# Kernel tuning notes

Hardware: AMD Instinct MI355X
Metric: run time of the kernel (lower is better)

Reference implementation:

```python
import jax, jax.numpy as jnp
import numpy as np

L, B, S, D, F, E, V, H = 4, 4, 1024, 768, 3072, 4, 256, 12
DH = D // H
TOPK = 2


def _ln(x, g, b, eps=1e-5):
    m = x.mean(-1, keepdims=True)
    v = ((x - m) ** 2).mean(-1, keepdims=True)
    return (x - m) * jax.lax.rsqrt(v + eps) * g + b


def setup_inputs() -> dict:
    key = jax.random.key(0)
    ks = iter(jax.random.split(key, 40))
    w = lambda shape, s=0.02: jax.random.normal(next(ks), shape, jnp.float32) * s
    inp = {
        'text': jax.random.randint(next(ks), (B, S), 0, V),
        'embed': w((V, D)),
        'conv_w': w((D, D, 3)),
        'conv_b': jnp.zeros((D,), jnp.float32),
        'Wq': w((L, D, D)), 'bq': jnp.zeros((L, D), jnp.float32),
        'Wk': w((L, D, D)), 'bk': jnp.zeros((L, D), jnp.float32),
        'Wv': w((L, D, D)), 'bv': jnp.zeros((L, D), jnp.float32),
        'Wo': w((L, D, D)), 'bo': jnp.zeros((L, D), jnp.float32),
        'rw': w((L, D, E)), 'rb': jnp.zeros((L, E), jnp.float32),
        'ew1': w((L, E, D, F)), 'eb1': jnp.zeros((L, E, F), jnp.float32),
        'ew2': w((L, E, F, D)), 'eb2': jnp.zeros((L, E, D), jnp.float32),
        'ln1g': jnp.ones((L, D), jnp.float32), 'ln1b': jnp.zeros((L, D), jnp.float32),
        'ln2g': jnp.ones((L, D), jnp.float32), 'ln2b': jnp.zeros((L, D), jnp.float32),
        'lnfg': jnp.ones((D,), jnp.float32), 'lnfb': jnp.zeros((D,), jnp.float32),
        'outw': w((D, V)), 'outb': jnp.zeros((V,), jnp.float32),
    }
    return inp


def _forward(text, embed, conv_w, conv_b, Wq, bq, Wk, bk, Wv, bv, Wo, bo,
             rw, rb, ew1, eb1, ew2, eb2, ln1g, ln1b, ln2g, ln2b, lnfg, lnfb, outw, outb):
    # --- morfo-semantic tokenizer: embedding + depthwise-ish conv1d residual ---
    x = embed[text]  # [B,S,D]
    xt = x.transpose(0, 2, 1)  # [B,D,S]
    y = jax.lax.conv_general_dilated(xt, conv_w, (1,), 'SAME',
                                     dimension_numbers=('NCH', 'OIH', 'NCH'))
    x = x + jax.nn.gelu(y.transpose(0, 2, 1) + conv_b)

    scale = 1.0 / np.sqrt(DH).astype(np.float32)
    for i in range(L):
        # --- multi-head self-attention (pre-norm residual) ---
        h = _ln(x, ln1g[i], ln1b[i])
        q = (h @ Wq[i] + bq[i]).reshape(B, S, H, DH).transpose(0, 2, 1, 3)
        k = (h @ Wk[i] + bk[i]).reshape(B, S, H, DH).transpose(0, 2, 1, 3)
        v = (h @ Wv[i] + bv[i]).reshape(B, S, H, DH).transpose(0, 2, 1, 3)
        a = jax.nn.softmax(jnp.einsum('bhqd,bhkd->bhqk', q, k) * scale, axis=-1)
        o = jnp.einsum('bhqk,bhkd->bhqd', a, v).transpose(0, 2, 1, 3).reshape(B, S, D)
        x = x + (o @ Wo[i] + bo[i])

        # --- top-2 mixture-of-experts (pre-norm residual) ---
        h = _ln(x, ln2g[i], ln2b[i]).reshape(B * S, D)  # [T,D]
        probs = jax.nn.softmax(h @ rw[i] + rb[i], axis=-1)  # [T,E]
        topv, topi = jax.lax.top_k(probs, TOPK)  # [T,2]
        gate_w = topv / topv.sum(-1, keepdims=True)  # renormalized top-k gates
        gate = (jax.nn.one_hot(topi, E, dtype=h.dtype) * gate_w[..., None]).sum(1)  # [T,E]
        h1 = jax.nn.gelu(jnp.einsum('td,edf->tef', h, ew1[i]) + eb1[i])  # [T,E,F]
        h2 = jnp.einsum('tef,efd->ted', h1, ew2[i]) + eb2[i]  # [T,E,D]
        moe_out = jnp.einsum('te,ted->td', gate, h2)
        x = x + moe_out.reshape(B, S, D)

    x = _ln(x, lnfg, lnfb)
    return x @ outw + outb  # logits [B,S,V]


def reference(text, embed, conv_w, conv_b, Wq, bq, Wk, bk, Wv, bv, Wo, bo,
              rw, rb, ew1, eb1, ew2, eb2, ln1g, ln1b, ln2g, ln2b, lnfg, lnfb, outw, outb):
    return _forward(text, embed, conv_w, conv_b, Wq, bq, Wk, bk, Wv, bv, Wo, bo,
                    rw, rb, ew1, eb1, ew2, eb2, ln1g, ln1b, ln2g, ln2b, lnfg, lnfb, outw, outb)
```

## Files before the change

### kernel.cpp

```cpp
#include <hip/hip_runtime.h>
#include <math.h>

#define L_ 4
#define B_ 4
#define S_ 1024
#define D_ 768
#define F_ 3072
#define E_ 4
#define V_ 256
#define H_ 12
#define DH_ 64
#define T_ (B_*S_)
#define QKV_LD (3*D_)

typedef __attribute__((ext_vector_type(8))) __bf16 bf16x8;
typedef __attribute__((ext_vector_type(4))) float f32x4;
typedef __attribute__((ext_vector_type(8))) unsigned short u16x8;

__device__ __forceinline__ ushort f2bf(float x) {
    union { float f; unsigned int u; } c; c.f = x;
    unsigned int u = c.u;
    unsigned int r = (u + 0x7fffu + ((u >> 16) & 1u)) >> 16;
    return (ushort)r;
}
__device__ __forceinline__ float bf2f(ushort u) {
    union { unsigned int u; float f; } c; c.u = ((unsigned int)u) << 16;
    return c.f;
}
__device__ __forceinline__ void split3(float v, ushort& h, ushort& l, ushort& q) {
    h = f2bf(v);
    float r1 = v - bf2f(h);
    l = f2bf(r1);
    float r2 = r1 - bf2f(l);
    q = f2bf(r2);
}

__device__ __forceinline__ float gelu_f(float x) {
    return 0.5f * x * (1.f + tanhf(0.7978845608028654f * (x + 0.044715f * x * x * x)));
}

__global__ __launch_bounds__(256) void embed_pad_k(const int* __restrict__ text,
                                                   const float* __restrict__ embed,
                                                   ushort* __restrict__ xpH,
                                                   ushort* __restrict__ xpL,
                                                   ushort* __restrict__ xpQ) {
    int idx = blockIdx.x * 256 + threadIdx.x;
    const int tot = B_ * (S_ + 2) * D_;
    if (idx >= tot) return;
    int d = idx % D_;
    int sp = (idx / D_) % (S_ + 2);
    int b = idx / (D_ * (S_ + 2));
    float v = 0.f;
    if (sp >= 1 && sp <= S_) {
        int tok = text[b * S_ + sp - 1];
        v = embed[(long)tok * D_ + d];
    }
    ushort h, l, q; split3(v, h, l, q);
    xpH[idx] = h; xpL[idx] = l; xpQ[idx] = q;
}

__global__ __launch_bounds__(256) void repack_conv_k(const float* __restrict__ w,
                                                     ushort* __restrict__ cH,
                                                     ushort* __restrict__ cL,
                                                     ushort* __restrict__ cQ) {
    int idx = blockIdx.x * 256 + threadIdx.x;
    if (idx >= D_ * 3 * D_) return;
    int o = idx / (3 * D_);
    int r = idx % (3 * D_);
    int wi = r / D_;
    int i = r % D_;
    float v = w[((long)o * D_ + i) * 3 + wi];
    ushort h, l, q; split3(v, h, l, q);
    cH[idx] = h; cL[idx] = l; cQ[idx] = q;
}

__global__ __launch_bounds__(256) void conv_rows_k(int* __restrict__ r) {
    int t = blockIdx.x * 256 + threadIdx.x;
    if (t < T_) r[t] = t + 2 * (t / S_);
}

__global__ void zero_cnt_k(int* c) { if (threadIdx.x < L_ * E_) c[threadIdx.x] = 0; }

__global__ void concat3_k(const float* __restrict__ a, const float* __restrict__ b,
                          const float* __restrict__ c, float* __restrict__ o) {
    int t = blockIdx.x * 256 + threadIdx.x;
    if (t < D_) o[t] = a[t];
    else if (t < 2 * D_) o[t] = b[t - D_];
    else if (t < 3 * D_) o[t] = c[t - 2 * D_];
}

__global__ __launch_bounds__(256) void tr4_split_k(const float* __restrict__ s0,
                                                   const float* __restrict__ s1,
                                                   const float* __restrict__ s2,
                                                   const float* __restrict__ s3,
                                                   ushort* __restrict__ dH,
                                                   ushort* __restrict__ dL,
                                                   ushort* __restrict__ dQ,
                                                   int K, int N, long dstStride) {
    int z = blockIdx.z;
    const float* src = (z == 0) ? s0 : (z == 1) ? s1 : (z == 2) ? s2 : s3;
    dH += (long)z * dstStride;
    dL += (long)z * dstStride;
    dQ += (long)z * dstStride;
    __shared__ float tile[32][33];
    int tx = threadIdx.x & 31, ty = threadIdx.x >> 5;
    int n = blockIdx.x * 32 + tx;
    int k0 = blockIdx.y * 32;
    #pragma unroll
    for (int r = ty; r < 32; r += 8)
        tile[r][tx] = src[(long)(k0 + r) * N + n];
    __syncthreads();
    int k = k0 + tx;
    long nb = (long)blockIdx.x * 32;
    #pragma unroll
    for (int r = ty; r < 32; r += 8) {
        float v = tile[tx][r];
        ushort h, l, q; split3(v, h, l, q);
        dH[(nb + r) * K + k] = h;
        dL[(nb + r) * K + k] = l;
        dQ[(nb + r) * K + k] = q;
    }
}

__global__ __launch_bounds__(256) void ln_k(const float* __restrict__ x,
                                            const float* __restrict__ g,
                                            const float* __restrict__ bb,
                                            ushort* __restrict__ oH,
                                            ushort* __restrict__ oL,
                                            ushort* __restrict__ oQ) {
    __shared__ float red[256];
    int row = blockIdx.x, tid = threadIdx.x;
    const float* xr = x + (long)row * D_;
    float v0 = xr[tid], v1 = xr[tid + 256], v2 = xr[tid + 512];
    red[tid] = v0 + v1 + v2; __syncthreads();
    for (int off = 128; off; off >>= 1) { if (tid < off) red[tid] += red[tid + off]; __syncthreads(); }
    float mean = red[0] * (1.f / D_);
    __syncthreads();
    float d0 = v0 - mean, d1 = v1 - mean, d2 = v2 - mean;
    red[tid] = d0 * d0 + d1 * d1 + d2 * d2; __syncthreads();
    for (int off = 128; off; off >>= 1) { if (tid < off) red[tid] += red[tid + off]; __syncthreads(); }
    float rs = rsqrtf(red[0] * (1.f / D_) + 1e-5f);
    long base = (long)row * D_;
    float y0 = d0 * rs * g[tid]       + bb[tid];
    float y1 = d1 * rs * g[tid + 256] + bb[tid + 256];
    float y2 = d2 * rs * g[tid + 512] + bb[tid + 512];
    ushort h, l, q;
    split3(y0, h, l, q); oH[base + tid]       = h; oL[base + tid]       = l; oQ[base + tid]       = q;
    split3(y1, h, l, q); oH[base + tid + 256] = h; oL[base + tid + 256] = l; oQ[base + tid + 256] = q;
    split3(y2, h, l, q); oH[base + tid + 512] = h; oL[base + tid + 512] = l; oQ[base + tid + 512] = q;
}

__global__ __launch_bounds__(256) void mfma_gemm_k(
    const ushort* __restrict__ AH, const ushort* __restrict__ AL, const ushort* __restrict__ AQ,
    const ushort* __restrict__ BH, const ushort* __restrict__ BL, const ushort* __restrict__ BQ,
    const float* __restrict__ bias,
    const float* __restrict__ resid,
    const ushort* __restrict__ rH, const ushort* __restrict__ rL, const ushort* __restrict__ rQ,
    float* __restrict__ C, ushort* __restrict__ CH, ushort* __restrict__ CL, ushort* __restrict__ CQ,
    const int* __restrict__ a_rows, const int* __restrict__ res_rows,
    const int* __restrict__ m_ptr,
    int M, int N, int K, int lda, int ldc, int act,
    const int* __restrict__ scat_rows, const float* __restrict__ scat_scale)
{
    int Meff = m_ptr ? *m_ptr : M;
    int m0 = blockIdx.y * 128, n0 = blockIdx.x * 128;
    if (m0 >= Meff) return;
    int Kc = K / gridDim.z;
    int kbeg = blockIdx.z * Kc;
    int kend = kbeg + Kc;

    int lane = threadIdx.x & 63;
    int wave = threadIdx.x >> 6;
    int wm = wave >> 1, wn = wave & 1;
    int lr = lane & 15;
    int g  = lane >> 4;

    long aoff[4];
    #pragma unroll
    for (int m = 0; m < 4; ++m) {
        int grow = m0 + wm * 64 + m * 16 + lr;
        int gr = grow < Meff ? grow : (Meff - 1);
        int r = a_rows ? a_rows[gr] : gr;
        aoff[m] = (long)r * lda + g * 8;
    }
    long boff[4];
    #pragma unroll
    for (int n = 0; n < 4; ++n) {
        int bcol = n0 + wn * 64 + n * 16 + lr;
        boff[n] = (long)bcol * K + g * 8;
    }

    f32x4 acc[4][4];
    #pragma unroll
    for (int m = 0; m < 4; ++m)
        #pragma unroll
        for (int n = 0; n < 4; ++n)
            acc[m][n] = (f32x4){0.f, 0.f, 0.f, 0.f};

    for (int k0 = kbeg; k0 < kend; k0 += 32) {
        bf16x8 ah[4], al[4], aq[4];
        #pragma unroll
        for (int m = 0; m < 4; ++m) {
            ah[m] = *reinterpret_cast<const bf16x8*>(AH + aoff[m] + k0);
            al[m] = *reinterpret_cast<const bf16x8*>(AL + aoff[m] + k0);
            aq[m] = *reinterpret_cast<const bf16x8*>(AQ + aoff[m] + k0);
        }
        #pragma unroll
        for (int n = 0; n < 4; ++n) {
            bf16x8 bh = *reinterpret_cast<const bf16x8*>(BH + boff[n] + k0);
            bf16x8 bl = *reinterpret_cast<const bf16x8*>(BL + boff[n] + k0);
            bf16x8 bq = *reinterpret_cast<const bf16x8*>(BQ + boff[n] + k0);
            #pragma unroll
            for (int m = 0; m < 4; ++m) {
                acc[m][n] = __builtin_amdgcn_mfma_f32_16x16x32_bf16(ah[m], bh, acc[m][n], 0, 0, 0);
                acc[m][n] = __builtin_amdgcn_mfma_f32_16x16x32_bf16(ah[m], bl, acc[m][n], 0, 0, 0);
                acc[m][n] = __builtin_amdgcn_mfma_f32_16x16x32_bf16(al[m], bh, acc[m][n], 0, 0, 0);
                acc[m][n] = __builtin_amdgcn_mfma_f32_16x16x32_bf16(al[m], bl, acc[m][n], 0, 0, 0);
                acc[m][n] = __builtin_amdgcn_mfma_f32_16x16x32_bf16(ah[m], bq, acc[m][n], 0, 0, 0);
                acc[m][n] = __builtin_amdgcn_mfma_f32_16x16x32_bf16(aq[m], bh, acc[m][n], 0, 0, 0);
            }
        }
    }

    #pragma unroll
    for (int m = 0; m < 4; ++m) {
        #pragma unroll
        for (int rr = 0; rr < 4; ++rr) {
            int row = m0 + wm * 64 + m * 16 + g * 4 + rr;
            if (row >= Meff) continue;
            #pragma unroll
            for (int n = 0; n < 4; ++n) {
                int col = n0 + wn * 64 + n * 16 + lr;
                float v = acc[m][n][rr];
                if (bias && blockIdx.z == 0) v += bias[col];
                if (act == 1) v = gelu_f(v);
                if (scat_rows) {
                    int t = scat_rows[row];
                    atomicAdd(&C[(long)t * ldc + col], scat_scale[row] * v);
                } else {
                    if (resid) {
                        int rq = res_rows ? res_rows[row] : row;
                        v += resid[(long)rq * ldc + col];
                    } else if (rH) {
                        int rq = res_rows ? res_rows[row] : row;
                        long off = (long)rq * ldc + col;
                        v += bf2f(rH[off]) + bf2f(rL[off]) + bf2f(rQ[off]);
                    }
                    if (CH) {
                        long off = (long)row * ldc + col;
                        ushort hh, ll, qq; split3(v, hh, ll, qq);
                        CH[off] = hh; CL[off] = ll; CQ[off] = qq;
                    } else {
                        C[(long)row * ldc + col] = v;
                    }
                }
            }
        }
    }
}

#define FA_PAD 68
__global__ __launch_bounds__(256) void flash_attn_k(const float* __restrict__ QKV,
                                                    ushort* __restrict__ OH,
                                                    ushort* __restrict__ OL,
                                                    ushort* __restrict__ OQ) {
    __shared__ float Qt[64][FA_PAD];
    __shared__ float KP[64][FA_PAD];
    __shared__ float Vs[64][FA_PAD];
    int blk = blockIdx.x;
    int qt = blk & 15;
    int h  = (blk >> 4) % H_;
    int b  = blk / (16 * H_);
    int q0 = qt * 64;
    long baseq = ((long)b * S_) * QKV_LD + h * DH_;
    int tid = threadIdx.x;
    int tx = tid & 15, ty = tid >> 4;
    int j = tid >> 2, c0 = (tid & 3) * 16;

    {
        const float* qp = QKV + baseq + (long)(q0 + j) * QKV_LD + c0;
        #pragma unroll
        for (int m = 0; m < 16; m += 4) {
            float4 v = *(const float4*)(qp + m);
            Qt[c0 + m + 0][j] = v.x; Qt[c0 + m + 1][j] = v.y;
            Qt[c0 + m + 2][j] = v.z; Qt[c0 + m + 3][j] = v.w;
        }
    }
    float o[4][4] = {};
    float mprev[4] = {-1e30f, -1e30f, -1e30f, -1e30f};
    float l[4] = {0.f, 0.f, 0.f, 0.f};

    for (int k0 = 0; k0 < S_; k0 += 64) {
        __syncthreads();
        {
            const float* kp = QKV + baseq + D_ + (long)(k0 + j) * QKV_LD + c0;
            #pragma unroll
            for (int m = 0; m < 16; m += 4) {
                float4 v = *(const float4*)(kp + m);
                KP[c0 + m + 0][j] = v.x; KP[c0 + m + 1][j] = v.y;
                KP[c0 + m + 2][j] = v.z; KP[c0 + m + 3][j] = v.w;
            }
            const float* vp = QKV + baseq + 2 * D_ + (long)(k0 + j) * QKV_LD + c0;
            #pragma unroll
            for (int m = 0; m < 16; m += 4) {
                *(float4*)&Vs[j][c0 + m] = *(const float4*)(vp + m);
            }
        }
        __syncthreads();
        float s[4][4] = {};
        #pragma unroll 8
        for (int d = 0; d < 64; ++d) {
            float4 qv = *(float4*)&Qt[d][ty * 4];
            float4 kv = *(float4*)&KP[d][tx * 4];
            s[0][0] += qv.x * kv.x; s[0][1] += qv.x * kv.y; s[0][2] += qv.x * kv.z; s[0][3] += qv.x * kv.w;
            s[1][0] += qv.y * kv.x; s[1][1] += qv.y * kv.y; s[1][2] += qv.y * kv.z; s[1][3] += qv.y * kv.w;
            s[2][0] += qv.z * kv.x; s[2][1] += qv.z * kv.y; s[2][2] += qv.z * kv.z; s[2][3] += qv.z * kv.w;
            s[3][0] += qv.w * kv.x; s[3][1] += qv.w * kv.y; s[3][2] += qv.w * kv.z; s[3][3] += qv.w * kv.w;
        }
        float alpha[4];
        #pragma unroll
        for (int i = 0; i < 4; ++i) {
            s[i][0] *= 0.125f; s[i][1] *= 0.125f; s[i][2] *= 0.125f; s[i][3] *= 0.125f;
            float mloc = fmaxf(fmaxf(s[i][0], s[i][1]), fmaxf(s[i][2], s[i][3]));
            #pragma unroll
            for (int off = 1; off < 16; off <<= 1) mloc = fmaxf(mloc, __shfl_xor(mloc, off));
            float mnew = fmaxf(mprev[i], mloc);
            alpha[i] = __expf(mprev[i] - mnew);
            s[i][0] = __expf(s[i][0] - mnew); s[i][1] = __expf(s[i][1] - mnew);
            s[i][2] = __expf(s[i][2] - mnew); s[i][3] = __expf(s[i][3] - mnew);
            float rs = s[i][0] + s[i][1] + s[i][2] + s[i][3];
            #pragma unroll
            for (int off = 1; off < 16; off <<= 1) rs += __shfl_xor(rs, off);
            l[i] = l[i] * alpha[i] + rs;
            mprev[i] = mnew;
            o[i][0] *= alpha[i]; o[i][1] *= alpha[i]; o[i][2] *= alpha[i]; o[i][3] *= alpha[i];
        }
        __syncthreads();
        #pragma unroll
        for (int i = 0; i < 4; ++i)
            *(float4*)&KP[ty * 4 + i][tx * 4] = make_float4(s[i][0], s[i][1], s[i][2], s[i][3]);
        __syncthreads();
        #pragma unroll 4
        for (int kk = 0; kk < 64; kk += 4) {
            float4 pr[4];
            #pragma unroll
            for (int i = 0; i < 4; ++i) pr[i] = *(float4*)&KP[ty * 4 + i][kk];
            #pragma unroll
            for (int e = 0; e < 4; ++e) {
                float4 vv = *(float4*)&Vs[kk + e][tx * 4];
                float pe0 = e == 0 ? pr[0].x : e == 1 ? pr[0].y : e == 2 ? pr[0].z : pr[0].w;
                float pe1 = e == 0 ? pr[1].x : e == 1 ? pr[1].y : e == 2 ? pr[1].z : pr[1].w;
                float pe2 = e == 0 ? pr[2].x : e == 1 ? pr[2].y : e == 2 ? pr[2].z : pr[2].w;
                float pe3 = e == 0 ? pr[3].x : e == 1 ? pr[3].y : e == 2 ? pr[3].z : pr[3].w;
                o[0][0] += pe0 * vv.x; o[0][1] += pe0 * vv.y; o[0][2] += pe0 * vv.z; o[0][3] += pe0 * vv.w;
                o[1][0] += pe1 * vv.x; o[1][1] += pe1 * vv.y; o[1][2] += pe1 * vv.z; o[1][3] += pe1 * vv.w;
                o[2][0] += pe2 * vv.x; o[2][1] += pe2 * vv.y; o[2][2] += pe2 * vv.z; o[2][3] += pe2 * vv.w;
                o[3][0] += pe3 * vv.x; o[3][1] += pe3 * vv.y; o[3][2] += pe3 * vv.z; o[3][3] += pe3 * vv.w;
            }
        }
    }
    long baseo = ((long)b * S_) * D_ + h * DH_;
    #pragma unroll
    for (int i = 0; i < 4; ++i) {
        float inv = 1.f / l[i];
        ushort4 hv, lv, qv;
        float v0 = o[i][0] * inv, v1 = o[i][1] * inv, v2 = o[i][2] * inv, v3 = o[i][3] * inv;
        split3(v0, hv.x, lv.x, qv.x);
        split3(v1, hv.y, lv.y, qv.y);
        split3(v2, hv.z, lv.z, qv.z);
        split3(v3, hv.w, lv.w, qv.w);
        long off = baseo + (long)(q0 + ty * 4 + i) * D_ + tx * 4;
        *(ushort4*)(OH + off) = hv;
        *(ushort4*)(OL + off) = lv;
        *(ushort4*)(OQ + off) = qv;
    }
}

__global__ __launch_bounds__(256) void router_fused_k(const ushort* __restrict__ HH,
                                                      const ushort* __restrict__ HL,
                                                      const ushort* __restrict__ HQ,
                                                      const float* __restrict__ rw,
                                                      const float* __restrict__ rb,
                                                      int* __restrict__ cnt,
                                                      int* __restrict__ list,
                                                      float* __restrict__ gate_slot) {
    __shared__ float rws[D_ * E_];
    int tid = threadIdx.x;
    for (int idx = tid; idx < D_ * E_; idx += 256) rws[idx] = rw[idx];
    __syncthreads();
    int tok = blockIdx.x * 64 + (tid >> 2);
    int e = tid & 3;
    const ushort* hh = HH + (long)tok * D_;
    const ushort* hl = HL + (long)tok * D_;
    const ushort* hq = HQ + (long)tok * D_;
    float s = rb[e];
    for (int d0 = 0; d0 < D_; d0 += 8) {
        u16x8 vh = *reinterpret_cast<const u16x8*>(hh + d0);
        u16x8 vl = *reinterpret_cast<const u16x8*>(hl + d0);
        u16x8 vq = *reinterpret_cast<const u16x8*>(hq + d0);
        #pragma unroll
        for (int jj = 0; jj < 8; ++jj) {
            float hv = bf2f((ushort)vh[jj]) + bf2f((ushort)vl[jj]) + bf2f((ushort)vq[jj]);
            s += hv * rws[(d0 + jj) * E_ + e];
        }
    }
    int lane = tid & 63;
    int bl = lane & ~3;
    float l0 = __shfl(s, bl + 0), l1 = __shfl(s, bl + 1);
    float l2 = __shfl(s, bl + 2), l3 = __shfl(s, bl + 3);
    if (e == 0) {
        float m = fmaxf(fmaxf(l0, l1), fmaxf(l2, l3));
        float p[4] = { __expf(l0 - m), __expf(l1 - m), __expf(l2 - m), __expf(l3 - m) };
        int i0 = 0; float v0p = p[0];
        #pragma unroll
        for (int q = 1; q < 4; ++q) if (p[q] > v0p) { v0p = p[q]; i0 = q; }
        int i1 = -1; float v1p = -1.f;
        #pragma unroll
        for (int q = 0; q < 4; ++q) { if (q == i0) continue; if (p[q] > v1p) { v1p = p[q]; i1 = q; } }
        float g0 = v0p / (v0p + v1p), g1 = v1p / (v0p + v1p);
        int pos0 = atomicAdd(&cnt[i0], 1);
        list[i0 * T_ + pos0] = tok; gate_slot[i0 * T_ + pos0] = g0;
        int pos1 = atomicAdd(&cnt[i1], 1);
        list[i1 * T_ + pos1] = tok; gate_slot[i1 * T_ + pos1] = g1;
    }
}

extern "C" void kernel_launch(void* const* d_in, const int* in_sizes, int n_in,
                              void* d_out, int out_size, void* d_ws, size_t ws_size,
                              hipStream_t stream) {
    const int*   text   = (const int*)  d_in[0];
    const float* embed  = (const float*)d_in[1];
    const float* conv_w = (const float*)d_in[2];
    const float* conv_b = (const float*)d_in[3];
    const float* Wq = (const float*)d_in[4],  *bq = (const float*)d_in[5];
    const float* Wk = (const float*)d_in[6],  *bk = (const float*)d_in[7];
    const float* Wv = (const float*)d_in[8],  *bv = (const float*)d_in[9];
    const float* Wo = (const float*)d_in[10], *bo = (const float*)d_in[11];
    const float* rw = (const float*)d_in[12], *rb = (const float*)d_in[13];
    const float* ew1 = (const float*)d_in[14], *eb1 = (const float*)d_in[15];
    const float* ew2 = (const float*)d_in[16], *eb2 = (const float*)d_in[17];
    const float* ln1g = (const float*)d_in[18], *ln1b = (const float*)d_in[19];
    const float* ln2g = (const float*)d_in[20], *ln2b = (const float*)d_in[21];
    const float* lnfg = (const float*)d_in[22], *lnfb = (const float*)d_in[23];
    const float* outw = (const float*)d_in[24], *outb = (const float*)d_in[25];
    float* out = (float*)d_out;
    (void)ws_size; (void)in_sizes; (void)n_in; (void)out_size;

    const size_t XP = (size_t)B_ * (S_ + 2) * D_;
    const size_t TD = (size_t)T_ * D_;
    const size_t TF = (size_t)T_ * F_;
    const size_t W4 = (size_t)4 * D_ * D_;
    const size_t CW = (size_t)D_ * 3 * D_;
    const size_t VD = (size_t)V_ * D_;
    const size_t DF = (size_t)D_ * F_;
    const size_t BIG_FL = 3 * TF / 2;

    float* BIGf = (float*)d_ws;
    ushort* BIGu = (ushort*)BIGf;
    ushort* xpH = BIGu;            ushort* xpL = xpH + XP;  ushort* xpQ = xpL + XP;
    ushort* cwH = BIGu + 3 * XP;   ushort* cwL = cwH + CW;  ushort* cwQ = cwL + CW;
    float*  qkv = BIGf;
    ushort* obH = BIGu + 2 * ((size_t)T_ * 3 * D_) / 2 * 0 + 18874368;
    ushort* obL = obH + TD;        ushort* obQ = obL + TD;
    ushort* w4H = BIGu + 28311552; ushort* w4L = w4H + W4;  ushort* w4Q = w4L + W4;
    ushort* owH = BIGu;            ushort* owL = owH + VD;  ushort* owQ = owL + VD;
    ushort* h1H = BIGu;            ushort* h1L = h1H + TF;  ushort* h1Q = h1L + TF;

    float* x     = BIGf + BIG_FL;
    ushort* hH   = (ushort*)(x + TD);
    ushort* hL   = hH + TD;
    ushort* hQ   = hL + TD;
    float* e1base = x + TD + 3 * TD / 2;
    ushort* e1H = (ushort*)e1base; ushort* e1L = e1H + DF; ushort* e1Q = e1L + DF;
    float* e2base = e1base + 3 * DF / 2;
    ushort* e2H = (ushort*)e2base; ushort* e2L = e2H + DF; ushort* e2Q = e2L + DF;
    float* qkvb = e2base + 3 * DF / 2;
    int* conv_rows = (int*)(qkvb + 3 * D_);
    int* list      = conv_rows + T_;
    float* gate_slot = (float*)(list + E_ * T_);
    int* cnt       = (int*)(gate_slot + E_ * T_);

    zero_cnt_k<<<1, 64, 0, stream>>>(cnt);
    embed_pad_k<<<(B_ * (S_ + 2) * D_ + 255) / 256, 256, 0, stream>>>(text, embed, xpH, xpL, xpQ);
    repack_conv_k<<<(3 * D_ * D_ + 255) / 256, 256, 0, stream>>>(conv_w, cwH, cwL, cwQ);
    conv_rows_k<<<(T_ + 255) / 256, 256, 0, stream>>>(conv_rows);
    mfma_gemm_k<<<dim3(D_ / 128, T_ / 128, 1), 256, 0, stream>>>(
        xpH, xpL, xpQ, cwH, cwL, cwQ, conv_b, nullptr,
        xpH + D_, xpL + D_, xpQ + D_,
        x, nullptr, nullptr, nullptr,
        conv_rows, conv_rows, nullptr, T_, D_, 3 * D_, D_, D_, 1, nullptr, nullptr);

    const long DD = (long)D_ * D_;
    for (int i = 0; i < L_; ++i) {
        ln_k<<<T_, 256, 0, stream>>>(x, ln1g + i * D_, ln1b + i * D_, hH, hL, hQ);
        tr4_split_k<<<dim3(D_ / 32, D_ / 32, 4), 256, 0, stream>>>(
            Wq + i * DD, Wk + i * DD, Wv + i * DD, Wo + i * DD, w4H, w4L, w4Q, D_, D_, DD);
        concat3_k<<<9, 256, 0, stream>>>(bq + i * D_, bk + i * D_, bv + i * D_, qkvb);
        mfma_gemm_k<<<dim3(3 * D_ / 128, T_ / 128, 1), 256, 0, stream>>>(
            hH, hL, hQ, w4H, w4L, w4Q, qkvb, nullptr, nullptr, nullptr, nullptr,
            qkv, nullptr, nullptr, nullptr,
            nullptr, nullptr, nullptr, T_, 3 * D_, D_, D_, 3 * D_, 0, nullptr, nullptr);
        flash_attn_k<<<B_ * H_ * (S_ / 64), 256, 0, stream>>>(qkv, obH, obL, obQ);
        mfma_gemm_k<<<dim3(D_ / 128, T_ / 128, 1), 256, 0, stream>>>(
            obH, obL, obQ, w4H + 3 * W4 / 4 * 0 + 3 * DD, w4L + 3 * DD, w4Q + 3 * DD,
            bo + i * D_, x, nullptr, nullptr, nullptr,
            x, nullptr, nullptr, nullptr,
            nullptr, nullptr, nullptr, T_, D_, D_, D_, D_, 0, nullptr, nullptr);
        ln_k<<<T_, 256, 0, stream>>>(x, ln2g + i * D_, ln2b + i * D_, hH, hL, hQ);
        router_fused_k<<<T_ / 64, 256, 0, stream>>>(
            hH, hL, hQ, rw + (long)i * D_ * E_, rb + i * E_, cnt + i * E_, list, gate_slot);
        for (int e = 0; e < E_; ++e) {
            const float* w1 = ew1 + ((long)i * E_ + e) * D_ * F_;
            const float* w2 = ew2 + ((long)i * E_ + e) * F_ * D_;
            tr4_split_k<<<dim3(F_ / 32, D_ / 32, 1), 256, 0, stream>>>(
                w1, w1, w1, w1, e1H, e1L, e1Q, D_, F_, 0);
            mfma_gemm_k<<<dim3(F_ / 128, T_ / 128, 1), 256, 0, stream>>>(
                hH, hL, hQ, e1H, e1L, e1Q, eb1 + ((long)i * E_ + e) * F_, nullptr, nullptr, nullptr, nullptr,
                nullptr, h1H, h1L, h1Q,
                list + e * T_, nullptr, cnt + i * E_ + e, T_, F_, D_, D_, F_, 1, nullptr, nullptr);
            tr4_split_k<<<dim3(D_ / 32, F_ / 32, 1), 256, 0, stream>>>(
                w2, w2, w2, w2, e2H, e2L, e2Q, F_, D_, 0);
            mfma_gemm_k<<<dim3(D_ / 128, T_ / 128, 4), 256, 0, stream>>>(
                h1H, h1L, h1Q, e2H, e2L, e2Q, eb2 + ((long)i * E_ + e) * D_, nullptr, nullptr, nullptr, nullptr,
                x, nullptr, nullptr, nullptr,
                nullptr, nullptr, cnt + i * E_ + e, T_, D_, F_, F_, D_, 0,
                list + e * T_, gate_slot + e * T_);
        }
    }
    ln_k<<<T_, 256, 0, stream>>>(x, lnfg, lnfb, hH, hL, hQ);
    tr4_split_k<<<dim3(V_ / 32, D_ / 32, 1), 256, 0, stream>>>(
        outw, outw, outw, outw, owH, owL, owQ, D_, V_, 0);
    mfma_gemm_k<<<dim3(V_ / 128, T_ / 128, 1), 256, 0, stream>>>(
        hH, hL, hQ, owH, owL, owQ, outb, nullptr, nullptr, nullptr, nullptr,
        out, nullptr, nullptr, nullptr,
        nullptr, nullptr, nullptr, T_, V_, D_, D_, V_, 0, nullptr, nullptr);
}
```

Baseline: 9.193 ms.

## Switch GEMM operand splitting from 3-way bf16 to 2-way scaled fp16

Every GEMM operand was stored as three bf16 parts and multiplied with six MFMAs per tile. It is now stored as a 2-term fp16 hi/lo split, with power-of-two prescaling to keep values in fp16 range, and needs three fp16 MFMAs into two accumulators. This removes half the MFMA work and a third of the operand memory traffic and storage. The change also remaps workgroups across XCDs and adds a two-waves-per-SIMD launch bound. In exchange, fp16 has less exponent range than bf16, so small values in the hi/lo residual may lose accuracy.

After: 7.890 ms. 1.17x faster.

```diff
diff --git a/kernel.cpp b/kernel.cpp
--- a/kernel.cpp
+++ b/kernel.cpp
@@ -13,26 +13,19 @@
 #define T_ (B_*S_)
 #define QKV_LD (3*D_)
 
-typedef __attribute__((ext_vector_type(8))) __bf16 bf16x8;
+typedef __attribute__((ext_vector_type(8))) _Float16 f16x8;
 typedef __attribute__((ext_vector_type(4))) float f32x4;
 typedef __attribute__((ext_vector_type(8))) unsigned short u16x8;
 
-__device__ __forceinline__ ushort f2bf(float x) {
-    union { float f; unsigned int u; } c; c.f = x;
-    unsigned int u = c.u;
-    unsigned int r = (u + 0x7fffu + ((u >> 16) & 1u)) >> 16;
-    return (ushort)r;
-}
-__device__ __forceinline__ float bf2f(ushort u) {
-    union { unsigned int u; float f; } c; c.u = ((unsigned int)u) << 16;
-    return c.f;
-}
-__device__ __forceinline__ void split3(float v, ushort& h, ushort& l, ushort& q) {
-    h = f2bf(v);
-    float r1 = v - bf2f(h);
-    l = f2bf(r1);
-    float r2 = r1 - bf2f(l);
-    q = f2bf(r2);
+__device__ __forceinline__ void split2(float v, ushort& h, ushort& l) {
+    _Float16 hh = (_Float16)v;
+    float r = (v - (float)hh) * 2048.0f;
+    _Float16 ll = (_Float16)r;
+    union { _Float16 x; ushort u; } a, b; a.x = hh; b.x = ll;
+    h = a.u; l = b.u;
+}
+__device__ __forceinline__ float h2f(ushort u) {
+    union { _Float16 x; ushort u; } c; c.u = u; return (float)c.x;
 }
 
 __device__ __forceinline__ float gelu_f(float x) {
@@ -42,8 +35,7 @@
 __global__ __launch_bounds__(256) void embed_pad_k(const int* __restrict__ text,
                                                    const float* __restrict__ embed,
                                                    ushort* __restrict__ xpH,
-                                                   ushort* __restrict__ xpL,
-                                                   ushort* __restrict__ xpQ) {
+                                                   ushort* __restrict__ xpL) {
     int idx = blockIdx.x * 256 + threadIdx.x;
     const int tot = B_ * (S_ + 2) * D_;
     if (idx >= tot) return;
@@ -55,14 +47,13 @@
         int tok = text[b * S_ + sp - 1];
         v = embed[(long)tok * D_ + d];
     }
-    ushort h, l, q; split3(v, h, l, q);
-    xpH[idx] = h; xpL[idx] = l; xpQ[idx] = q;
+    ushort h, l; split2(v * 64.0f, h, l);
+    xpH[idx] = h; xpL[idx] = l;
 }
 
 __global__ __launch_bounds__(256) void repack_conv_k(const float* __restrict__ w,
                                                      ushort* __restrict__ cH,
-                                                     ushort* __restrict__ cL,
-                                                     ushort* __restrict__ cQ) {
+                                                     ushort* __restrict__ cL) {
     int idx = blockIdx.x * 256 + threadIdx.x;
     if (idx >= D_ * 3 * D_) return;
     int o = idx / (3 * D_);
@@ -70,8 +61,8 @@
     int wi = r / D_;
     int i = r % D_;
     float v = w[((long)o * D_ + i) * 3 + wi];
-    ushort h, l, q; split3(v, h, l, q);
-    cH[idx] = h; cL[idx] = l; cQ[idx] = q;
+    ushort h, l; split2(v * 64.0f, h, l);
+    cH[idx] = h; cL[idx] = l;
 }
 
 __global__ __launch_bounds__(256) void conv_rows_k(int* __restrict__ r) {
@@ -95,13 +86,11 @@
                                                    const float* __restrict__ s3,
                                                    ushort* __restrict__ dH,
                                                    ushort* __restrict__ dL,
-                                                   ushort* __restrict__ dQ,
                                                    int K, int N, long dstStride) {
     int z = blockIdx.z;
     const float* src = (z == 0) ? s0 : (z == 1) ? s1 : (z == 2) ? s2 : s3;
     dH += (long)z * dstStride;
     dL += (long)z * dstStride;
-    dQ += (long)z * dstStride;
     __shared__ float tile[32][33];
     int tx = threadIdx.x & 31, ty = threadIdx.x >> 5;
     int n = blockIdx.x * 32 + tx;
@@ -114,11 +103,9 @@
     long nb = (long)blockIdx.x * 32;
     #pragma unroll
     for (int r = ty; r < 32; r += 8) {
-        float v = tile[tx][r];
-        ushort h, l, q; split3(v, h, l, q);
+        ushort h, l; split2(tile[tx][r] * 64.0f, h, l);
         dH[(nb + r) * K + k] = h;
         dL[(nb + r) * K + k] = l;
-        dQ[(nb + r) * K + k] = q;
     }
 }
 
@@ -126,8 +113,7 @@
                                             const float* __restrict__ g,
                                             const float* __restrict__ bb,
                                             ushort* __restrict__ oH,
-                                            ushort* __restrict__ oL,
-                                            ushort* __restrict__ oQ) {
+                                            ushort* __restrict__ oL) {
     __shared__ float red[256];
     int row = blockIdx.x, tid = threadIdx.x;
     const float* xr = x + (long)row * D_;
@@ -144,26 +130,35 @@
     float y0 = d0 * rs * g[tid]       + bb[tid];
     float y1 = d1 * rs * g[tid + 256] + bb[tid + 256];
     float y2 = d2 * rs * g[tid + 512] + bb[tid + 512];
-    ushort h, l, q;
-    split3(y0, h, l, q); oH[base + tid]       = h; oL[base + tid]       = l; oQ[base + tid]       = q;
-    split3(y1, h, l, q); oH[base + tid + 256] = h; oL[base + tid + 256] = l; oQ[base + tid + 256] = q;
-    split3(y2, h, l, q); oH[base + tid + 512] = h; oL[base + tid + 512] = l; oQ[base + tid + 512] = q;
-}
-
-__global__ __launch_bounds__(256) void mfma_gemm_k(
-    const ushort* __restrict__ AH, const ushort* __restrict__ AL, const ushort* __restrict__ AQ,
-    const ushort* __restrict__ BH, const ushort* __restrict__ BL, const ushort* __restrict__ BQ,
+    ushort h, l;
+    split2(y0, h, l); oH[base + tid]       = h; oL[base + tid]       = l;
+    split2(y1, h, l); oH[base + tid + 256] = h; oL[base + tid + 256] = l;
+    split2(y2, h, l); oH[base + tid + 512] = h; oL[base + tid + 512] = l;
+}
+
+__global__ __launch_bounds__(256, 2) void mfma_gemm_k(
+    const ushort* __restrict__ AH, const ushort* __restrict__ AL,
+    const ushort* __restrict__ BH, const ushort* __restrict__ BL,
     const float* __restrict__ bias,
     const float* __restrict__ resid,
-    const ushort* __restrict__ rH, const ushort* __restrict__ rL, const ushort* __restrict__ rQ,
-    float* __restrict__ C, ushort* __restrict__ CH, ushort* __restrict__ CL, ushort* __restrict__ CQ,
+    const ushort* __restrict__ rH, const ushort* __restrict__ rL, float resInvScale,
+    float* __restrict__ C, ushort* __restrict__ CH, ushort* __restrict__ CL,
     const int* __restrict__ a_rows, const int* __restrict__ res_rows,
     const int* __restrict__ m_ptr,
-    int M, int N, int K, int lda, int ldc, int act,
+    int M, int N, int K, int lda, int ldc, int act, float invScale,
     const int* __restrict__ scat_rows, const float* __restrict__ scat_scale)
 {
+    int nbx = gridDim.x, nby = gridDim.y;
+    int nwg = nbx * nby;
+    int orig = blockIdx.y * nbx + blockIdx.x;
+    int qq = nwg >> 3, rr8 = nwg & 7;
+    int xcd = orig & 7, sidx = orig >> 3;
+    int wg = (xcd < rr8 ? xcd * (qq + 1) : rr8 * (qq + 1) + (xcd - rr8) * qq) + sidx;
+    int bx = wg / nby;
+    int by = wg % nby;
+
     int Meff = m_ptr ? *m_ptr : M;
-    int m0 = blockIdx.y * 128, n0 = blockIdx.x * 128;
+    int m0 = by * 128, n0 = bx * 128;
     if (m0 >= Meff) return;
     int Kc = K / gridDim.z;
     int kbeg = blockIdx.z * Kc;
@@ -190,34 +185,31 @@
         boff[n] = (long)bcol * K + g * 8;
     }
 
-    f32x4 acc[4][4];
+    f32x4 acc0[4][4], acc1[4][4];
     #pragma unroll
     for (int m = 0; m < 4; ++m)
         #pragma unroll
-        for (int n = 0; n < 4; ++n)
-            acc[m][n] = (f32x4){0.f, 0.f, 0.f, 0.f};
+        for (int n = 0; n < 4; ++n) {
+            acc0[m][n] = (f32x4){0.f, 0.f, 0.f, 0.f};
+            acc1[m][n] = (f32x4){0.f, 0.f, 0.f, 0.f};
+        }
 
     for (int k0 = kbeg; k0 < kend; k0 += 32) {
-        bf16x8 ah[4], al[4], aq[4];
+        f16x8 ah[4], al[4];
         #pragma unroll
         for (int m = 0; m < 4; ++m) {
-            ah[m] = *reinterpret_cast<const bf16x8*>(AH + aoff[m] + k0);
-            al[m] = *reinterpret_cast<const bf16x8*>(AL + aoff[m] + k0);
-            aq[m] = *reinterpret_cast<const bf16x8*>(AQ + aoff[m] + k0);
+            ah[m] = *reinterpret_cast<const f16x8*>(AH + aoff[m] + k0);
+            al[m] = *reinterpret_cast<const f16x8*>(AL + aoff[m] + k0);
         }
         #pragma unroll
         for (int n = 0; n < 4; ++n) {
-            bf16x8 bh = *reinterpret_cast<const bf16x8*>(BH + boff[n] + k0);
-            bf16x8 bl = *reinterpret_cast<const bf16x8*>(BL + boff[n] + k0);
-            bf16x8 bq = *reinterpret_cast<const bf16x8*>(BQ + boff[n] + k0);
+            f16x8 bh = *reinterpret_cast<const f16x8*>(BH + boff[n] + k0);
+            f16x8 bl = *reinterpret_cast<const f16x8*>(BL + boff[n] + k0);
             #pragma unroll
             for (int m = 0; m < 4; ++m) {
-                acc[m][n] = __builtin_amdgcn_mfma_f32_16x16x32_bf16(ah[m], bh, acc[m][n], 0, 0, 0);
-                acc[m][n] = __builtin_amdgcn_mfma_f32_16x16x32_bf16(ah[m], bl, acc[m][n], 0, 0, 0);
-                acc[m][n] = __builtin_amdgcn_mfma_f32_16x16x32_bf16(al[m], bh, acc[m][n], 0, 0, 0);
-                acc[m][n] = __builtin_amdgcn_mfma_f32_16x16x32_bf16(al[m], bl, acc[m][n], 0, 0, 0);
-                acc[m][n] = __builtin_amdgcn_mfma_f32_16x16x32_bf16(ah[m], bq, acc[m][n], 0, 0, 0);
-                acc[m][n] = __builtin_amdgcn_mfma_f32_16x16x32_bf16(aq[m], bh, acc[m][n], 0, 0, 0);
+                acc0[m][n] = __builtin_amdgcn_mfma_f32_16x16x32_f16(ah[m], bh, acc0[m][n], 0, 0, 0);
+                acc1[m][n] = __builtin_amdgcn_mfma_f32_16x16x32_f16(ah[m], bl, acc1[m][n], 0, 0, 0);
+                acc1[m][n] = __builtin_amdgcn_mfma_f32_16x16x32_f16(al[m], bh, acc1[m][n], 0, 0, 0);
             }
         }
     }
@@ -231,7 +223,7 @@
             #pragma unroll
             for (int n = 0; n < 4; ++n) {
                 int col = n0 + wn * 64 + n * 16 + lr;
-                float v = acc[m][n][rr];
+                float v = (acc0[m][n][rr] + acc1[m][n][rr] * (1.0f / 2048.0f)) * invScale;
                 if (bias && blockIdx.z == 0) v += bias[col];
                 if (act == 1) v = gelu_f(v);
                 if (scat_rows) {
@@ -244,12 +236,12 @@
                     } else if (rH) {
                         int rq = res_rows ? res_rows[row] : row;
                         long off = (long)rq * ldc + col;
-                        v += bf2f(rH[off]) + bf2f(rL[off]) + bf2f(rQ[off]);
+                        v += (h2f(rH[off]) + h2f(rL[off]) * (1.0f / 2048.0f)) * resInvScale;
                     }
                     if (CH) {
                         long off = (long)row * ldc + col;
-                        ushort hh, ll, qq; split3(v, hh, ll, qq);
-                        CH[off] = hh; CL[off] = ll; CQ[off] = qq;
+                        ushort hh, ll; split2(v, hh, ll);
+                        CH[off] = hh; CL[off] = ll;
                     } else {
                         C[(long)row * ldc + col] = v;
                     }
@@ -262,8 +254,7 @@
 #define FA_PAD 68
 __global__ __launch_bounds__(256) void flash_attn_k(const float* __restrict__ QKV,
                                                     ushort* __restrict__ OH,
-                                                    ushort* __restrict__ OL,
-                                                    ushort* __restrict__ OQ) {
+                                                    ushort* __restrict__ OL) {
     __shared__ float Qt[64][FA_PAD];
     __shared__ float KP[64][FA_PAD];
     __shared__ float Vs[64][FA_PAD];
@@ -363,22 +354,19 @@
     #pragma unroll
     for (int i = 0; i < 4; ++i) {
         float inv = 1.f / l[i];
-        ushort4 hv, lv, qv;
-        float v0 = o[i][0] * inv, v1 = o[i][1] * inv, v2 = o[i][2] * inv, v3 = o[i][3] * inv;
-        split3(v0, hv.x, lv.x, qv.x);
-        split3(v1, hv.y, lv.y, qv.y);
-        split3(v2, hv.z, lv.z, qv.z);
-        split3(v3, hv.w, lv.w, qv.w);
+        ushort4 hv, lv;
+        split2(o[i][0] * inv, hv.x, lv.x);
+        split2(o[i][1] * inv, hv.y, lv.y);
+        split2(o[i][2] * inv, hv.z, lv.z);
+        split2(o[i][3] * inv, hv.w, lv.w);
         long off = baseo + (long)(q0 + ty * 4 + i) * D_ + tx * 4;
         *(ushort4*)(OH + off) = hv;
         *(ushort4*)(OL + off) = lv;
-        *(ushort4*)(OQ + off) = qv;
     }
 }
 
 __global__ __launch_bounds__(256) void router_fused_k(const ushort* __restrict__ HH,
                                                       const ushort* __restrict__ HL,
-                                                      const ushort* __restrict__ HQ,
                                                       const float* __restrict__ rw,
                                                       const float* __restrict__ rb,
                                                       int* __restrict__ cnt,
@@ -392,15 +380,13 @@
     int e = tid & 3;
     const ushort* hh = HH + (long)tok * D_;
     const ushort* hl = HL + (long)tok * D_;
-    const ushort* hq = HQ + (long)tok * D_;
     float s = rb[e];
     for (int d0 = 0; d0 < D_; d0 += 8) {
         u16x8 vh = *reinterpret_cast<const u16x8*>(hh + d0);
         u16x8 vl = *reinterpret_cast<const u16x8*>(hl + d0);
-        u16x8 vq = *reinterpret_cast<const u16x8*>(hq + d0);
         #pragma unroll
         for (int jj = 0; jj < 8; ++jj) {
-            float hv = bf2f((ushort)vh[jj]) + bf2f((ushort)vl[jj]) + bf2f((ushort)vq[jj]);
+            float hv = h2f((ushort)vh[jj]) + h2f((ushort)vl[jj]) * (1.0f / 2048.0f);
             s += hv * rws[(d0 + jj) * E_ + e];
         }
     }
@@ -453,85 +439,85 @@
     const size_t CW = (size_t)D_ * 3 * D_;
     const size_t VD = (size_t)V_ * D_;
     const size_t DF = (size_t)D_ * F_;
-    const size_t BIG_FL = 3 * TF / 2;
+    const size_t QKV_FL = (size_t)T_ * 3 * D_;
+    const size_t BIG_FL = QKV_FL + (2 * TD + 2 * W4) / 2;
 
     float* BIGf = (float*)d_ws;
     ushort* BIGu = (ushort*)BIGf;
-    ushort* xpH = BIGu;            ushort* xpL = xpH + XP;  ushort* xpQ = xpL + XP;
-    ushort* cwH = BIGu + 3 * XP;   ushort* cwL = cwH + CW;  ushort* cwQ = cwL + CW;
+    ushort* xpH = BIGu;               ushort* xpL = xpH + XP;
+    ushort* cwH = BIGu + 2 * XP;      ushort* cwL = cwH + CW;
     float*  qkv = BIGf;
-    ushort* obH = BIGu + 2 * ((size_t)T_ * 3 * D_) / 2 * 0 + 18874368;
-    ushort* obL = obH + TD;        ushort* obQ = obL + TD;
-    ushort* w4H = BIGu + 28311552; ushort* w4L = w4H + W4;  ushort* w4Q = w4L + W4;
-    ushort* owH = BIGu;            ushort* owL = owH + VD;  ushort* owQ = owL + VD;
-    ushort* h1H = BIGu;            ushort* h1L = h1H + TF;  ushort* h1Q = h1L + TF;
-
-    float* x     = BIGf + BIG_FL;
-    ushort* hH   = (ushort*)(x + TD);
-    ushort* hL   = hH + TD;
-    ushort* hQ   = hL + TD;
-    float* e1base = x + TD + 3 * TD / 2;
-    ushort* e1H = (ushort*)e1base; ushort* e1L = e1H + DF; ushort* e1Q = e1L + DF;
-    float* e2base = e1base + 3 * DF / 2;
-    ushort* e2H = (ushort*)e2base; ushort* e2L = e2H + DF; ushort* e2Q = e2L + DF;
-    float* qkvb = e2base + 3 * DF / 2;
+    ushort* obH = BIGu + 2 * QKV_FL;  ushort* obL = obH + TD;
+    ushort* w4H = obH + 2 * TD;       ushort* w4L = w4H + W4;
+    ushort* h1H = BIGu;               ushort* h1L = h1H + TF;
+    ushort* owH = BIGu;               ushort* owL = owH + VD;
+
+    float* x   = BIGf + BIG_FL;
+    ushort* hH = (ushort*)(x + TD);
+    ushort* hL = hH + TD;
+    float* aft = x + TD + TD;
+    ushort* e1H = (ushort*)aft;        ushort* e1L = e1H + DF;
+    ushort* e2H = e1H + 2 * DF;        ushort* e2L = e2H + DF;
+    float* qkvb = aft + DF + DF;
     int* conv_rows = (int*)(qkvb + 3 * D_);
     int* list      = conv_rows + T_;
     float* gate_slot = (float*)(list + E_ * T_);
     int* cnt       = (int*)(gate_slot + E_ * T_);
 
+    const float INV64 = 1.0f / 64.0f;
+    const float INV4096 = 1.0f / 4096.0f;
+
     zero_cnt_k<<<1, 64, 0, stream>>>(cnt);
-    embed_pad_k<<<(B_ * (S_ + 2) * D_ + 255) / 256, 256, 0, stream>>>(text, embed, xpH, xpL, xpQ);
-    repack_conv_k<<<(3 * D_ * D_ + 255) / 256, 256, 0, stream>>>(conv_w, cwH, cwL, cwQ);
+    embed_pad_k<<<(B_ * (S_ + 2) * D_ + 255) / 256, 256, 0, stream>>>(text, embed, xpH, xpL);
+    repack_conv_k<<<(3 * D_ * D_ + 255) / 256, 256, 0, stream>>>(conv_w, cwH, cwL);
     conv_rows_k<<<(T_ + 255) / 256, 256, 0, stream>>>(conv_rows);
     mfma_gemm_k<<<dim3(D_ / 128, T_ / 128, 1), 256, 0, stream>>>(
-        xpH, xpL, xpQ, cwH, cwL, cwQ, conv_b, nullptr,
-        xpH + D_, xpL + D_, xpQ + D_,
-        x, nullptr, nullptr, nullptr,
-        conv_rows, conv_rows, nullptr, T_, D_, 3 * D_, D_, D_, 1, nullptr, nullptr);
+        xpH, xpL, cwH, cwL, conv_b, nullptr,
+        xpH + D_, xpL + D_, INV64,
+        x, nullptr, nullptr,
+        conv_rows, conv_rows, nullptr, T_, D_, 3 * D_, D_, D_, 1, INV4096, nullptr, nullptr);
 
     const long DD = (long)D_ * D_;
     for (int i = 0; i < L_; ++i) {
-        ln_k<<<T_, 256, 0, stream>>>(x, ln1g + i * D_, ln1b + i * D_, hH, hL, hQ);
+        ln_k<<<T_, 256, 0, stream>>>(x, ln1g + i * D_, ln1b + i * D_, hH, hL);
         tr4_split_k<<<dim3(D_ / 32, D_ / 32, 4), 256, 0, stream>>>(
-            Wq + i * DD, Wk + i * DD, Wv + i * DD, Wo + i * DD, w4H, w4L, w4Q, D_, D_, DD);
+            Wq + i * DD, Wk + i * DD, Wv + i * DD, Wo + i * DD, w4H, w4L, D_, D_, DD);
         concat3_k<<<9, 256, 0, stream>>>(bq + i * D_, bk + i * D_, bv + i * D_, qkvb);
         mfma_gemm_k<<<dim3(3 * D_ / 128, T_ / 128, 1), 256, 0, stream>>>(
-            hH, hL, hQ, w4H, w4L, w4Q, qkvb, nullptr, nullptr, nullptr, nullptr,
-            qkv, nullptr, nullptr, nullptr,
-            nullptr, nullptr, nullptr, T_, 3 * D_, D_, D_, 3 * D_, 0, nullptr, nullptr);
-        flash_attn_k<<<B_ * H_ * (S_ / 64), 256, 0, stream>>>(qkv, obH, obL, obQ);
+            hH, hL, w4H, w4L, qkvb, nullptr, nullptr, nullptr, 0.f,
+            qkv, nullptr, nullptr,
+            nullptr, nullptr, nullptr, T_, 3 * D_, D_, D_, 3 * D_, 0, INV64, nullptr, nullptr);
+        flash_attn_k<<<B_ * H_ * (S_ / 64), 256, 0, stream>>>(qkv, obH, obL);
         mfma_gemm_k<<<dim3(D_ / 128, T_ / 128, 1), 256, 0, stream>>>(
-            obH, obL, obQ, w4H + 3 * W4 / 4 * 0 + 3 * DD, w4L + 3 * DD, w4Q + 3 * DD,
-            bo + i * D_, x, nullptr, nullptr, nullptr,
-            x, nullptr, nullptr, nullptr,
-            nullptr, nullptr, nullptr, T_, D_, D_, D_, D_, 0, nullptr, nullptr);
-        ln_k<<<T_, 256, 0, stream>>>(x, ln2g + i * D_, ln2b + i * D_, hH, hL, hQ);
+            obH, obL, w4H + 3 * DD, w4L + 3 * DD, bo + i * D_, x, nullptr, nullptr, 0.f,
+            x, nullptr, nullptr,
+            nullptr, nullptr, nullptr, T_, D_, D_, D_, D_, 0, INV64, nullptr, nullptr);
+        ln_k<<<T_, 256, 0, stream>>>(x, ln2g + i * D_, ln2b + i * D_, hH, hL);
         router_fused_k<<<T_ / 64, 256, 0, stream>>>(
-            hH, hL, hQ, rw + (long)i * D_ * E_, rb + i * E_, cnt + i * E_, list, gate_slot);
+            hH, hL, rw + (long)i * D_ * E_, rb + i * E_, cnt + i * E_, list, gate_slot);
         for (int e = 0; e < E_; ++e) {
             const float* w1 = ew1 + ((long)i * E_ + e) * D_ * F_;
             const float* w2 = ew2 + ((long)i * E_ + e) * F_ * D_;
             tr4_split_k<<<dim3(F_ / 32, D_ / 32, 1), 256, 0, stream>>>(
-                w1, w1, w1, w1, e1H, e1L, e1Q, D_, F_, 0);
+                w1, w1, w1, w1, e1H, e1L, D_, F_, 0);
             mfma_gemm_k<<<dim3(F_ / 128, T_ / 128, 1), 256, 0, stream>>>(
-                hH, hL, hQ, e1H, e1L, e1Q, eb1 + ((long)i * E_ + e) * F_, nullptr, nullptr, nullptr, nullptr,
-                nullptr, h1H, h1L, h1Q,
-                list + e * T_, nullptr, cnt + i * E_ + e, T_, F_, D_, D_, F_, 1, nullptr, nullptr);
+                hH, hL, e1H, e1L, eb1 + ((long)i * E_ + e) * F_, nullptr, nullptr, nullptr, 0.f,
+                nullptr, h1H, h1L,
+                list + e * T_, nullptr, cnt + i * E_ + e, T_, F_, D_, D_, F_, 1, INV64, nullptr, nullptr);
             tr4_split_k<<<dim3(D_ / 32, F_ / 32, 1), 256, 0, stream>>>(
-                w2, w2, w2, w2, e2H, e2L, e2Q, F_, D_, 0);
+                w2, w2, w2, w2, e2H, e2L, F_, D_, 0);
             mfma_gemm_k<<<dim3(D_ / 128, T_ / 128, 4), 256, 0, stream>>>(
-                h1H, h1L, h1Q, e2H, e2L, e2Q, eb2 + ((long)i * E_ + e) * D_, nullptr, nullptr, nullptr, nullptr,
-                x, nullptr, nullptr, nullptr,
-                nullptr, nullptr, cnt + i * E_ + e, T_, D_, F_, F_, D_, 0,
+                h1H, h1L, e2H, e2L, eb2 + ((long)i * E_ + e) * D_, nullptr, nullptr, nullptr, 0.f,
+                x, nullptr, nullptr,
+                nullptr, nullptr, cnt + i * E_ + e, T_, D_, F_, F_, D_, 0, INV64,
                 list + e * T_, gate_slot + e * T_);
         }
     }
-    ln_k<<<T_, 256, 0, stream>>>(x, lnfg, lnfb, hH, hL, hQ);
+    ln_k<<<T_, 256, 0, stream>>>(x, lnfg, lnfb, hH, hL);
     tr4_split_k<<<dim3(V_ / 32, D_ / 32, 1), 256, 0, stream>>>(
-        outw, outw, outw, outw, owH, owL, owQ, D_, V_, 0);
+        outw, outw, outw, outw, owH, owL, D_, V_, 0);
     mfma_gemm_k<<<dim3(V_ / 128, T_ / 128, 1), 256, 0, stream>>>(
-        hH, hL, hQ, owH, owL, owQ, outb, nullptr, nullptr, nullptr, nullptr,
-        out, nullptr, nullptr, nullptr,
-        nullptr, nullptr, nullptr, T_, V_, D_, D_, V_, 0, nullptr, nullptr);
-}
+        hH, hL, owH, owL, outb, nullptr, nullptr, nullptr, 0.f,
+        out, nullptr, nullptr,
+        nullptr, nullptr, nullptr, T_, V_, D_, D_, V_, 0, INV64, nullptr, nullptr);
+}
```
